# Kernel optimization log

Hardware: AMD Instinct MI355X
Metric: run time of the kernel (lower is better)

The kernel has to match this reference:

```python
import jax, jax.numpy as jnp
import numpy as np

EPS = 1e-8

def setup_inputs() -> dict:
    key = jax.random.key(0)
    ks = jax.random.split(key, 10)
    B, T, D = 128, 128, 512
    inp = {"joint": jax.random.normal(ks[0], (B, D), dtype=jnp.float32)}
    names = ["f00", "f01", "f02", "f10", "f11", "f12", "f20", "f21", "f22"]
    for n, k in zip(names, ks[1:]):
        inp[n] = jax.random.normal(k, (B, T, D), dtype=jnp.float32)
    inp["B"] = B
    return inp


def reference(joint, f00, f01, f02, f10, f11, f12, f20, f21, f22, B):
    # F: [N, N, B, T, D] with N = 3
    F = jnp.stack([
        jnp.stack([f00, f01, f02]),
        jnp.stack([f10, f11, f12]),
        jnp.stack([f20, f21, f22]),
    ])
    fmean = F.mean(axis=3)                                   # [N, N, B, D]
    num = jnp.einsum("bd,ijbd->ijb", joint, fmean)           # [N, N, B]
    denom = num.sum(axis=1, keepdims=True) + EPS             # [N, 1, B]
    b = num / denom                                          # [N, N, B]
    # intra-scale weighted sum: f_ii[i] = sum_j b[i,j] * F[i,j]
    f_ii = jnp.einsum("ijb,ijbtd->ibtd", b, F)               # [N, B, T, D]
    fii_mean = f_ii.mean(axis=2)                             # [N, B, D]
    num2 = jnp.einsum("bd,ibd->ib", joint, fii_mean)         # [N, B]
    denom2 = num2.sum(axis=0) + EPS                          # [B]
    lam = num2 / denom2                                      # [N, B]
    return jnp.einsum("ib,ibd->bd", lam, fii_mean)           # [B, D]
```

## Files before the change

### kernel.cpp

```cpp
#include <hip/hip_runtime.h>

#define EPS 1e-8f

typedef float f4 __attribute__((ext_vector_type(4)));

namespace {
constexpr int Bc = 128;
constexpr int Tc = 128;
constexpr int Dc = 512;
constexpr int D4 = Dc / 4;
constexpr int COLS_PER_TENSOR = Bc * D4;
constexpr int THREADS1 = 64;
constexpr int GRID1 = 9 * COLS_PER_TENSOR / THREADS1;
}

__global__ __launch_bounds__(64, 2) void hm_mean_kernel(
    const float* __restrict__ f0, const float* __restrict__ f1,
    const float* __restrict__ f2, const float* __restrict__ f3,
    const float* __restrict__ f4_, const float* __restrict__ f5,
    const float* __restrict__ f6, const float* __restrict__ f7,
    const float* __restrict__ f8, float* __restrict__ fmean)
{
    const float* fs[9] = {f0, f1, f2, f3, f4_, f5, f6, f7, f8};
    const int gid = blockIdx.x * THREADS1 + threadIdx.x;
    const int q   = gid >> 14;
    const int idx = gid & (COLS_PER_TENSOR - 1);
    const int b   = idx >> 7;
    const int d4  = idx & (D4 - 1);

    const f4* src = reinterpret_cast<const f4*>(fs[q])
                  + (size_t)b * Tc * D4 + d4;

    f4 acc[4];
    #pragma unroll
    for (int u = 0; u < 4; ++u) acc[u] = (f4){0.f, 0.f, 0.f, 0.f};

    for (int t0 = 0; t0 < Tc; t0 += 16) {
        f4 buf[16];
        #pragma unroll
        for (int u = 0; u < 16; ++u)
            buf[u] = src[(size_t)(t0 + u) * D4];
        #pragma unroll
        for (int u = 0; u < 16; ++u)
            acc[u & 3] += buf[u];
    }

    f4 r = (acc[0] + acc[1]) + (acc[2] + acc[3]);
    reinterpret_cast<f4*>(fmean)[(size_t)q * COLS_PER_TENSOR + idx] = r;
}

__global__ __launch_bounds__(256) void hm_final_kernel(
    const float* __restrict__ joint, const float* __restrict__ fmean,
    float* __restrict__ out)
{
    const int b    = blockIdx.x;
    const int tid  = threadIdx.x;
    const int lane = tid & 63;
    const int wave = tid >> 6;

    __shared__ float sm_red[4][9];
    __shared__ float sm_red2[4][3];
    __shared__ float sm_num[9];
    __shared__ float sm_num2[3];

    const float invT = 1.0f / (float)Tc;

    float jd[2];
    float fm[2][9];
    float pnum[9];
    #pragma unroll
    for (int q = 0; q < 9; ++q) pnum[q] = 0.f;

    #pragma unroll
    for (int r = 0; r < 2; ++r) {
        const int d = tid + r * 256;
        jd[r] = joint[(size_t)b * Dc + d];
        #pragma unroll
        for (int q = 0; q < 9; ++q) {
            fm[r][q] = fmean[((size_t)q * Bc + b) * Dc + d] * invT;
            pnum[q] += jd[r] * fm[r][q];
        }
    }

    #pragma unroll
    for (int q = 0; q < 9; ++q)
        #pragma unroll
        for (int off = 32; off > 0; off >>= 1)
            pnum[q] += __shfl_down(pnum[q], off, 64);
    if (lane == 0)
        #pragma unroll
        for (int q = 0; q < 9; ++q) sm_red[wave][q] = pnum[q];
    __syncthreads();
    if (tid < 9)
        sm_num[tid] = sm_red[0][tid] + sm_red[1][tid] + sm_red[2][tid] + sm_red[3][tid];
    __syncthreads();

    float num[9];
    #pragma unroll
    for (int q = 0; q < 9; ++q) num[q] = sm_num[q];
    float bw[3][3];
    #pragma unroll
    for (int i = 0; i < 3; ++i) {
        const float denom = num[i * 3] + num[i * 3 + 1] + num[i * 3 + 2] + EPS;
        const float rdenom = 1.0f / denom;
        #pragma unroll
        for (int j = 0; j < 3; ++j) bw[i][j] = num[i * 3 + j] * rdenom;
    }

    float fii[2][3];
    float pnum2[3] = {0.f, 0.f, 0.f};
    #pragma unroll
    for (int r = 0; r < 2; ++r)
        #pragma unroll
        for (int i = 0; i < 3; ++i) {
            fii[r][i] = bw[i][0] * fm[r][i * 3 + 0]
                      + bw[i][1] * fm[r][i * 3 + 1]
                      + bw[i][2] * fm[r][i * 3 + 2];
            pnum2[i] += jd[r] * fii[r][i];
        }

    #pragma unroll
    for (int i = 0; i < 3; ++i)
        #pragma unroll
        for (int off = 32; off > 0; off >>= 1)
            pnum2[i] += __shfl_down(pnum2[i], off, 64);
    if (lane == 0)
        #pragma unroll
        for (int i = 0; i < 3; ++i) sm_red2[wave][i] = pnum2[i];
    __syncthreads();
    if (tid < 3)
        sm_num2[tid] = sm_red2[0][tid] + sm_red2[1][tid] + sm_red2[2][tid] + sm_red2[3][tid];
    __syncthreads();

    const float denom2 = sm_num2[0] + sm_num2[1] + sm_num2[2] + EPS;
    const float rd2 = 1.0f / denom2;
    float lam[3];
    #pragma unroll
    for (int i = 0; i < 3; ++i) lam[i] = sm_num2[i] * rd2;

    #pragma unroll
    for (int r = 0; r < 2; ++r) {
        const int d = tid + r * 256;
        out[(size_t)b * Dc + d] =
            lam[0] * fii[r][0] + lam[1] * fii[r][1] + lam[2] * fii[r][2];
    }
}

extern "C" void kernel_launch(void* const* d_in, const int* in_sizes, int n_in,
                              void* d_out, int out_size, void* d_ws, size_t ws_size,
                              hipStream_t stream) {
    const float* joint = (const float*)d_in[0];
    const float* f[9];
    for (int q = 0; q < 9; ++q) f[q] = (const float*)d_in[1 + q];
    float* out = (float*)d_out;
    float* fmean = (float*)d_ws;

    hipLaunchKernelGGL(hm_mean_kernel, dim3(GRID1), dim3(THREADS1), 0, stream,
                       f[0], f[1], f[2], f[3], f[4], f[5], f[6], f[7], f[8], fmean);
    hipLaunchKernelGGL(hm_final_kernel, dim3(Bc), dim3(256), 0, stream,
                       joint, fmean, out);
}
```

Measured before the change: 53.52 us.

## Fuse mean and final kernels via per-batch atomic completion counter

Merges the two kernels into one. Each block writes its slice of the T-means, then bumps a per-batch atomic counter, and the last of the 18 producer blocks for that batch runs the weighting and output step with a single wave. This removes the second kernel launch and its dependency gap, but adds a memset launch, threadfences and atomics. It also serialises the tail work onto one 64-thread wave per batch.

```diff
diff --git a/kernel.cpp b/kernel.cpp
--- a/kernel.cpp
+++ b/kernel.cpp
@@ -12,14 +12,18 @@
 constexpr int COLS_PER_TENSOR = Bc * D4;
 constexpr int THREADS1 = 64;
 constexpr int GRID1 = 9 * COLS_PER_TENSOR / THREADS1;
+constexpr int PRODUCERS_PER_B = 18;
+constexpr size_t FMEAN_ELEMS = (size_t)9 * Bc * Dc;
 }
 
-__global__ __launch_bounds__(64, 2) void hm_mean_kernel(
+__global__ __launch_bounds__(64, 2) void hm_fused_kernel(
     const float* __restrict__ f0, const float* __restrict__ f1,
     const float* __restrict__ f2, const float* __restrict__ f3,
     const float* __restrict__ f4_, const float* __restrict__ f5,
     const float* __restrict__ f6, const float* __restrict__ f7,
-    const float* __restrict__ f8, float* __restrict__ fmean)
+    const float* __restrict__ f8, const float* __restrict__ joint,
+    float* __restrict__ fmean, unsigned int* __restrict__ cnt,
+    float* __restrict__ out)
 {
     const float* fs[9] = {f0, f1, f2, f3, f4_, f5, f6, f7, f8};
     const int gid = blockIdx.x * THREADS1 + threadIdx.x;
@@ -47,102 +51,76 @@
 
     f4 r = (acc[0] + acc[1]) + (acc[2] + acc[3]);
     reinterpret_cast<f4*>(fmean)[(size_t)q * COLS_PER_TENSOR + idx] = r;
-}
 
-__global__ __launch_bounds__(256) void hm_final_kernel(
-    const float* __restrict__ joint, const float* __restrict__ fmean,
-    float* __restrict__ out)
-{
-    const int b    = blockIdx.x;
-    const int tid  = threadIdx.x;
-    const int lane = tid & 63;
-    const int wave = tid >> 6;
+    __threadfence();
+    int old = 0;
+    if (threadIdx.x == 0)
+        old = (int)atomicAdd(&cnt[b], 1u);
+    old = __shfl(old, 0, 64);
+    if (old != PRODUCERS_PER_B - 1) return;
+    __threadfence();
 
-    __shared__ float sm_red[4][9];
-    __shared__ float sm_red2[4][3];
-    __shared__ float sm_num[9];
-    __shared__ float sm_num2[3];
-
+    const int t = threadIdx.x;
     const float invT = 1.0f / (float)Tc;
 
-    float jd[2];
-    float fm[2][9];
+    float jd[8];
     float pnum[9];
     #pragma unroll
-    for (int q = 0; q < 9; ++q) pnum[q] = 0.f;
-
+    for (int q2 = 0; q2 < 9; ++q2) pnum[q2] = 0.f;
     #pragma unroll
-    for (int r = 0; r < 2; ++r) {
-        const int d = tid + r * 256;
-        jd[r] = joint[(size_t)b * Dc + d];
+    for (int k = 0; k < 8; ++k) {
+        const int d = k * 64 + t;
+        jd[k] = joint[(size_t)b * Dc + d];
         #pragma unroll
-        for (int q = 0; q < 9; ++q) {
-            fm[r][q] = fmean[((size_t)q * Bc + b) * Dc + d] * invT;
-            pnum[q] += jd[r] * fm[r][q];
-        }
+        for (int q2 = 0; q2 < 9; ++q2)
+            pnum[q2] += jd[k] * fmean[((size_t)q2 * Bc + b) * Dc + d];
     }
-
     #pragma unroll
-    for (int q = 0; q < 9; ++q)
+    for (int q2 = 0; q2 < 9; ++q2)
         #pragma unroll
         for (int off = 32; off > 0; off >>= 1)
-            pnum[q] += __shfl_down(pnum[q], off, 64);
-    if (lane == 0)
-        #pragma unroll
-        for (int q = 0; q < 9; ++q) sm_red[wave][q] = pnum[q];
-    __syncthreads();
-    if (tid < 9)
-        sm_num[tid] = sm_red[0][tid] + sm_red[1][tid] + sm_red[2][tid] + sm_red[3][tid];
-    __syncthreads();
+            pnum[q2] += __shfl_xor(pnum[q2], off, 64);
 
-    float num[9];
-    #pragma unroll
-    for (int q = 0; q < 9; ++q) num[q] = sm_num[q];
     float bw[3][3];
     #pragma unroll
     for (int i = 0; i < 3; ++i) {
-        const float denom = num[i * 3] + num[i * 3 + 1] + num[i * 3 + 2] + EPS;
-        const float rdenom = 1.0f / denom;
-        #pragma unroll
-        for (int j = 0; j < 3; ++j) bw[i][j] = num[i * 3 + j] * rdenom;
+        const float n0 = pnum[i * 3] * invT, n1 = pnum[i * 3 + 1] * invT,
+                    n2 = pnum[i * 3 + 2] * invT;
+        const float rdenom = 1.0f / (n0 + n1 + n2 + EPS);
+        bw[i][0] = n0 * rdenom; bw[i][1] = n1 * rdenom; bw[i][2] = n2 * rdenom;
     }
 
-    float fii[2][3];
+    float fii[8][3];
     float pnum2[3] = {0.f, 0.f, 0.f};
     #pragma unroll
-    for (int r = 0; r < 2; ++r)
+    for (int k = 0; k < 8; ++k) {
+        const int d = k * 64 + t;
+        float fm[9];
+        #pragma unroll
+        for (int q2 = 0; q2 < 9; ++q2)
+            fm[q2] = fmean[((size_t)q2 * Bc + b) * Dc + d] * invT;
         #pragma unroll
         for (int i = 0; i < 3; ++i) {
-            fii[r][i] = bw[i][0] * fm[r][i * 3 + 0]
-                      + bw[i][1] * fm[r][i * 3 + 1]
-                      + bw[i][2] * fm[r][i * 3 + 2];
-            pnum2[i] += jd[r] * fii[r][i];
+            fii[k][i] = bw[i][0] * fm[i * 3 + 0]
+                      + bw[i][1] * fm[i * 3 + 1]
+                      + bw[i][2] * fm[i * 3 + 2];
+            pnum2[i] += jd[k] * fii[k][i];
         }
-
+    }
     #pragma unroll
     for (int i = 0; i < 3; ++i)
         #pragma unroll
         for (int off = 32; off > 0; off >>= 1)
-            pnum2[i] += __shfl_down(pnum2[i], off, 64);
-    if (lane == 0)
-        #pragma unroll
-        for (int i = 0; i < 3; ++i) sm_red2[wave][i] = pnum2[i];
-    __syncthreads();
-    if (tid < 3)
-        sm_num2[tid] = sm_red2[0][tid] + sm_red2[1][tid] + sm_red2[2][tid] + sm_red2[3][tid];
-    __syncthreads();
+            pnum2[i] += __shfl_xor(pnum2[i], off, 64);
 
-    const float denom2 = sm_num2[0] + sm_num2[1] + sm_num2[2] + EPS;
-    const float rd2 = 1.0f / denom2;
-    float lam[3];
-    #pragma unroll
-    for (int i = 0; i < 3; ++i) lam[i] = sm_num2[i] * rd2;
+    const float rd2 = 1.0f / (pnum2[0] + pnum2[1] + pnum2[2] + EPS);
+    const float lam0 = pnum2[0] * rd2, lam1 = pnum2[1] * rd2, lam2 = pnum2[2] * rd2;
 
     #pragma unroll
-    for (int r = 0; r < 2; ++r) {
-        const int d = tid + r * 256;
+    for (int k = 0; k < 8; ++k) {
+        const int d = k * 64 + t;
         out[(size_t)b * Dc + d] =
-            lam[0] * fii[r][0] + lam[1] * fii[r][1] + lam[2] * fii[r][2];
+            lam0 * fii[k][0] + lam1 * fii[k][1] + lam2 * fii[k][2];
     }
 }
 
@@ -152,11 +130,13 @@
     const float* joint = (const float*)d_in[0];
     const float* f[9];
     for (int q = 0; q < 9; ++q) f[q] = (const float*)d_in[1 + q];
-    float* out = (float*)d_out;
+    float* out   = (float*)d_out;
     float* fmean = (float*)d_ws;
+    unsigned int* cnt = (unsigned int*)((char*)d_ws + FMEAN_ELEMS * sizeof(float));
 
-    hipLaunchKernelGGL(hm_mean_kernel, dim3(GRID1), dim3(THREADS1), 0, stream,
-                       f[0], f[1], f[2], f[3], f[4], f[5], f[6], f[7], f[8], fmean);
-    hipLaunchKernelGGL(hm_final_kernel, dim3(Bc), dim3(256), 0, stream,
-                       joint, fmean, out);
+    hipMemsetAsync(cnt, 0, Bc * sizeof(unsigned int), stream);
+
+    hipLaunchKernelGGL(hm_fused_kernel, dim3(GRID1), dim3(THREADS1), 0, stream,
+                       f[0], f[1], f[2], f[3], f[4], f[5], f[6], f[7], f[8],
+                       joint, fmean, cnt, out);
 }
```

Result: slower. 167.5 us (+213.1%).
